# Optimization experiments

Measured on AMD Instinct MI355X. Metric: run time of the kernel, lower is better.

## Reference

```python
import jax, jax.numpy as jnp
import numpy as np

K = 256
Q = 64
T = 500001  # length of return series r


def setup_inputs() -> dict:
    key = jax.random.key(0)
    k_r, k_b, k_w0, k_w = jax.random.split(key, 4)
    r = 0.01 * jax.random.normal(k_r, (T,), dtype=jnp.float32)
    a0 = jnp.float32(0.0)
    a1 = jnp.float32(0.0)
    raw_beta0 = jnp.float32(-4.0)
    raw_beta = (-4.0 + 0.1 * jax.random.normal(k_b, (K,))).astype(jnp.float32)
    raw_w0 = (-8.0 + 0.1 * jax.random.normal(k_w0, (K,))).astype(jnp.float32)
    raw_w = (-4.0 + 0.1 * jax.random.normal(k_w, (K, Q))).astype(jnp.float32)
    return {"r": r, "a0": a0, "a1": a1, "raw_beta0": raw_beta0,
            "raw_beta": raw_beta, "raw_w0": raw_w0, "raw_w": raw_w}


def reference(r, a0, a1, raw_beta0, raw_beta, raw_w0, raw_w):
    # AR(1) residuals
    u = r[1:] - a0 - a1 * r[:-1]          # [T-1]
    u2 = u * u                            # [T-1]
    n = u.shape[0]
    # init_u2 = unbiased variance of u2, repeated q times (torch.var default ddof=1)
    init_u2 = jnp.full((Q,), jnp.var(u2, ddof=1), dtype=u2.dtype)
    u2_full = jnp.concatenate([init_u2, u2])  # [q + T-1]
    # vectorized windowing: row t holds u2_full[t+q-1], ..., u2_full[t] (flipped window)
    t_idx = jnp.arange(n)[:, None]        # [n,1]
    lag_idx = jnp.arange(Q)[None, :]      # [1,q]
    idx = (Q + t_idx) - 1 - lag_idx       # [n,q]
    u2_lags = u2_full[idx]                # [n,q]
    # softplus-MLP volatility
    w0 = jax.nn.softplus(raw_w0)          # [k]
    w = jax.nn.softplus(raw_w)            # [k,q]
    h = jax.nn.relu(w0[None, :] + u2_lags @ w.T)  # [n,k]
    beta0 = jax.nn.softplus(raw_beta0)
    beta = jax.nn.softplus(raw_beta)      # [k]
    sigma2 = beta0 + h @ beta + 1e-8      # [n]
    # Gaussian negative log-likelihood
    nll = (0.5 * n * jnp.log(jnp.float32(2.0 * np.pi))
           + 0.5 * jnp.sum(jnp.log(sigma2))
           + 0.5 * jnp.sum(u2 / sigma2))
    return nll
```

## Files before the change

### kernel.cpp

```cpp
#include <hip/hip_runtime.h>
#include <math.h>

#define K_ 256
#define Q_ 64
#define NT 500000
#define NTILES (NT / 16)
#define TT_ 16
#define NBLK ((NT + 255) / 256)
#define GRID_MAIN ((NTILES + TT_ - 1) / TT_)
#define PREP_THREADS (16384 + 2 * K_)
#define PREP_BLOCKS ((PREP_THREADS + 255) / 256)

#define WS_BETA0  2
#define WS_U2B0   4
#define WS_U2B1   (WS_U2B0 + (Q_ + NT + 1) / 2)
#define WS_BPACK  (WS_U2B1 + (Q_ + NT + 1) / 2)
#define WS_W0     (WS_BPACK + 8192)
#define WS_BETA   (WS_W0 + K_)
#define WS_PART   (WS_BETA + K_)
#define WS_PART2  (WS_PART + 2048)
#define WS_OUT    (WS_PART2 + 2048)

typedef __attribute__((ext_vector_type(8))) __bf16 bf16x8;
typedef __attribute__((ext_vector_type(4))) float  f32x4;

__device__ __forceinline__ float softplusf(float x) {
    return (x > 20.f) ? x : log1pf(__expf(x));
}

__device__ __forceinline__ unsigned short f2bf(float f) {
    unsigned int u = __float_as_uint(f);
    u = u + 0x7FFFu + ((u >> 16) & 1u);
    return (unsigned short)(u >> 16);
}

__global__ void k_front(const float* __restrict__ r,
                        const float* __restrict__ a0p,
                        const float* __restrict__ a1p,
                        const float* __restrict__ raw_beta0,
                        const float* __restrict__ raw_beta,
                        const float* __restrict__ raw_w0,
                        const float* __restrict__ raw_w,
                        float* __restrict__ ws) {
    __shared__ float red[8];
    int bi = blockIdx.x - NBLK;
    if (bi < 0) {
        int i = blockIdx.x * blockDim.x + threadIdx.x;
        float a0 = a0p[0], a1 = a1p[0];
        float v = 0.f, v2 = 0.f;
        if (i < NT) {
            float u  = r[i + 1] - a0 - a1 * r[i];
            float u2 = u * u;
            unsigned short b = f2bf(u2);
            ((unsigned short*)(ws + WS_U2B0))[Q_ + i]     = b;
            ((unsigned short*)(ws + WS_U2B1))[Q_ + i - 1] = b;
            v = u2; v2 = u2 * u2;
        }
        #pragma unroll
        for (int off = 32; off > 0; off >>= 1) {
            v  += __shfl_down(v,  off, 64);
            v2 += __shfl_down(v2, off, 64);
        }
        int wv = threadIdx.x >> 6;
        if ((threadIdx.x & 63) == 0) { red[wv * 2] = v; red[wv * 2 + 1] = v2; }
        __syncthreads();
        if (threadIdx.x == 0) {
            ws[WS_PART  + blockIdx.x] = red[0] + red[2] + red[4] + red[6];
            ws[WS_PART2 + blockIdx.x] = red[1] + red[3] + red[5] + red[7];
        }
    } else {
        int idx = bi * 256 + threadIdx.x;
        if (idx < 16384) {
            int jj = idx & 7, l = (idx >> 3) & 63, s = (idx >> 9) & 1, kc = idx >> 10;
            int j    = 32 * s + 8 * (l >> 4) + jj;
            int kout = kc * 16 + (l & 15);
            ((unsigned short*)(ws + WS_BPACK))[idx] =
                f2bf(softplusf(raw_w[kout * Q_ + (Q_ - 1 - j)]));
        } else if (idx < 16384 + K_) {
            int k = idx - 16384;
            ws[WS_W0 + k] = softplusf(raw_w0[k]);
            if (k == 0) ws[WS_BETA0] = softplusf(raw_beta0[0]);
        } else if (idx < 16384 + 2 * K_) {
            int k = idx - (16384 + K_);
            ws[WS_BETA + k] = softplusf(raw_beta[k]);
        }
    }
}

__launch_bounds__(256, 4)
__global__ void k_main(const float* __restrict__ r,
                       const float* __restrict__ a0p,
                       const float* __restrict__ a1p,
                       float* __restrict__ ws) {
    __shared__ __align__(16) float sig[TT_ * 272];
    __shared__ float red[4];

    int tid = threadIdx.x;
    int l = tid & 63, w = tid >> 6;
    int m = l & 15, q = l >> 4;

    if (blockIdx.x == 0) {
        if (tid < 64) {
            float s1 = 0.f, s2 = 0.f;
            for (int p = tid; p < NBLK; p += 64) {
                s1 += ws[WS_PART  + p];
                s2 += ws[WS_PART2 + p];
            }
            #pragma unroll
            for (int mask = 1; mask < 64; mask <<= 1) {
                s1 += __shfl_xor(s1, mask, 64);
                s2 += __shfl_xor(s2, mask, 64);
            }
            float n   = (float)NT;
            float var = (s2 - s1 * s1 / n) / (n - 1.f);
            unsigned short b = f2bf(var);
            ((unsigned short*)(ws + WS_U2B0))[tid] = b;
            if (tid < Q_ - 1) ((unsigned short*)(ws + WS_U2B1))[tid] = b;
        }
        __syncthreads();
    }

    const unsigned short* bp = (const unsigned short*)(ws + WS_BPACK);
    float beta0v = ws[WS_BETA0];
    float a0 = a0p[0], a1 = a1p[0];

    bf16x8 Wf[4][2];
    f32x4 w0c[4], betc[4];
    #pragma unroll
    for (int i = 0; i < 4; ++i) {
        int kc = w * 4 + i;
        #pragma unroll
        for (int s = 0; s < 2; ++s)
            __builtin_memcpy(&Wf[i][s], bp + ((kc * 2 + s) * 64 + l) * 8, 16);
        w0c[i]  = *(const f32x4*)(ws + WS_W0   + kc * 16 + q * 4);
        betc[i] = *(const f32x4*)(ws + WS_BETA + kc * 16 + q * 4);
    }

    int par = m & 1;
    const char* abase = (const char*)(ws + (par ? WS_U2B1 : WS_U2B0));
    int tile0 = blockIdx.x * TT_;
    int aoff = (tile0 * 16 + m + 8 * q - par) * 2;

    bf16x8 U0, U1, U0n, U1n;
    __builtin_memcpy(&U0, abase + aoff, 16);
    __builtin_memcpy(&U1, abase + aoff + 64, 16);

    #pragma unroll 2
    for (int it = 0; it < TT_; ++it) {
        int anext = aoff + 32;
        __builtin_memcpy(&U0n, abase + anext, 16);
        __builtin_memcpy(&U1n, abase + anext + 64, 16);

        float p[4];
        #pragma unroll
        for (int i = 0; i < 4; ++i) {
            f32x4 acc = __builtin_amdgcn_mfma_f32_16x16x32_bf16(Wf[i][0], U0, w0c[i], 0, 0, 0);
            acc = __builtin_amdgcn_mfma_f32_16x16x32_bf16(Wf[i][1], U1, acc, 0, 0, 0);
            float pi;
            pi = betc[i][0] * fmaxf(acc[0], 0.f);
            pi = fmaf(betc[i][1], fmaxf(acc[1], 0.f), pi);
            pi = fmaf(betc[i][2], fmaxf(acc[2], 0.f), pi);
            pi = fmaf(betc[i][3], fmaxf(acc[3], 0.f), pi);
            p[i] = pi;
        }
        sig[it * 272 + tid] = (p[0] + p[1]) + (p[2] + p[3]);

        aoff = anext; U0 = U0n; U1 = U1n;
    }

    __syncthreads();

    int tile = tid >> 4, tt = tid & 15;
    const float* sp = &sig[tile * 272 + tt];
    float s = 0.f;
    #pragma unroll
    for (int wq = 0; wq < 16; ++wq) s += sp[wq * 16];
    float sg = beta0v + s + 1e-8f;
    int t = tile0 * 16 + tid;
    float val = 0.f;
    if (t < NT) {
        float u = r[t + 1] - a0 - a1 * r[t];
        val = __logf(sg) + u * u / sg;
    }

    #pragma unroll
    for (int mask = 1; mask < 64; mask <<= 1)
        val += __shfl_xor(val, mask, 64);
    if (l == 0) red[w] = val;
    __syncthreads();
    if (tid == 0)
        ws[WS_OUT + blockIdx.x] = red[0] + red[1] + red[2] + red[3];
}

__global__ void k_final(const float* __restrict__ ws, float* __restrict__ out) {
    __shared__ float red[4];
    int tid = threadIdx.x;
    float s = 0.f;
    for (int p = tid; p < GRID_MAIN; p += 256) s += ws[WS_OUT + p];
    #pragma unroll
    for (int mask = 1; mask < 64; mask <<= 1)
        s += __shfl_xor(s, mask, 64);
    if ((tid & 63) == 0) red[tid >> 6] = s;
    __syncthreads();
    if (tid == 0)
        out[0] = 0.5f * (float)NT * 1.8378770664093453f
               + 0.5f * (red[0] + red[1] + red[2] + red[3]);
}

extern "C" void kernel_launch(void* const* d_in, const int* in_sizes, int n_in,
                              void* d_out, int out_size, void* d_ws, size_t ws_size,
                              hipStream_t stream) {
    const float* r        = (const float*)d_in[0];
    const float* a0       = (const float*)d_in[1];
    const float* a1       = (const float*)d_in[2];
    const float* raw_b0   = (const float*)d_in[3];
    const float* raw_beta = (const float*)d_in[4];
    const float* raw_w0   = (const float*)d_in[5];
    const float* raw_w    = (const float*)d_in[6];
    float* out = (float*)d_out;
    float* ws  = (float*)d_ws;

    k_front<<<NBLK + PREP_BLOCKS, 256, 0, stream>>>(
        r, a0, a1, raw_b0, raw_beta, raw_w0, raw_w, ws);

    k_main<<<GRID_MAIN, 256, 0, stream>>>(r, a0, a1, ws);

    k_final<<<1, 256, 0, stream>>>(ws, out);
}
```

Baseline: 91.13 us.

## Switch main MFMA from 16x16x32 to 32x32x16 bf16 tiles

Reworks the main kernel to compute 32-timestep by 32-hidden-unit tiles with the 32x32x16 bf16 MFMA. Each wave now covers 64 hidden units across four K-steps, and the weight packing in the prep kernel is changed to match the new operand layout. Larger tiles mean fewer cross-lane partial sums and better operand reuse per instruction. In exchange, each thread holds 16-wide accumulator, bias and beta vectors, so register pressure rises and launch bounds drop from 4 to 3 blocks per SM.

```diff
diff --git a/kernel.cpp b/kernel.cpp
--- a/kernel.cpp
+++ b/kernel.cpp
@@ -4,10 +4,9 @@
 #define K_ 256
 #define Q_ 64
 #define NT 500000
-#define NTILES (NT / 16)
-#define TT_ 16
+#define TPB 256
 #define NBLK ((NT + 255) / 256)
-#define GRID_MAIN ((NTILES + TT_ - 1) / TT_)
+#define GRID_MAIN ((NT + TPB - 1) / TPB)
 #define PREP_THREADS (16384 + 2 * K_)
 #define PREP_BLOCKS ((PREP_THREADS + 255) / 256)
 
@@ -21,8 +20,9 @@
 #define WS_PART2  (WS_PART + 2048)
 #define WS_OUT    (WS_PART2 + 2048)
 
-typedef __attribute__((ext_vector_type(8))) __bf16 bf16x8;
-typedef __attribute__((ext_vector_type(4))) float  f32x4;
+typedef __attribute__((ext_vector_type(8)))  __bf16 bf16x8;
+typedef __attribute__((ext_vector_type(4)))  float  f32x4;
+typedef __attribute__((ext_vector_type(16))) float  f32x16;
 
 __device__ __forceinline__ float softplusf(float x) {
     return (x > 20.f) ? x : log1pf(__expf(x));
@@ -71,9 +71,9 @@
     } else {
         int idx = bi * 256 + threadIdx.x;
         if (idx < 16384) {
-            int jj = idx & 7, l = (idx >> 3) & 63, s = (idx >> 9) & 1, kc = idx >> 10;
-            int j    = 32 * s + 8 * (l >> 4) + jj;
-            int kout = kc * 16 + (l & 15);
+            int jj = idx & 7, l = (idx >> 3) & 63, kb = (idx >> 9) & 3, kc = idx >> 11;
+            int j    = kb * 16 + 8 * (l >> 5) + jj;
+            int kout = kc * 32 + (l & 31);
             ((unsigned short*)(ws + WS_BPACK))[idx] =
                 f2bf(softplusf(raw_w[kout * Q_ + (Q_ - 1 - j)]));
         } else if (idx < 16384 + K_) {
@@ -87,17 +87,17 @@
     }
 }
 
-__launch_bounds__(256, 4)
+__launch_bounds__(256, 3)
 __global__ void k_main(const float* __restrict__ r,
                        const float* __restrict__ a0p,
                        const float* __restrict__ a1p,
                        float* __restrict__ ws) {
-    __shared__ __align__(16) float sig[TT_ * 272];
+    __shared__ __align__(16) float sig[8 * 264];
     __shared__ float red[4];
 
     int tid = threadIdx.x;
     int l = tid & 63, w = tid >> 6;
-    int m = l & 15, q = l >> 4;
+    int tl = l & 31, hi = l >> 5;
 
     if (blockIdx.x == 0) {
         if (tid < 64) {
@@ -124,59 +124,70 @@
     float beta0v = ws[WS_BETA0];
     float a0 = a0p[0], a1 = a1p[0];
 
-    bf16x8 Wf[4][2];
-    f32x4 w0c[4], betc[4];
-    #pragma unroll
-    for (int i = 0; i < 4; ++i) {
-        int kc = w * 4 + i;
-        #pragma unroll
-        for (int s = 0; s < 2; ++s)
-            __builtin_memcpy(&Wf[i][s], bp + ((kc * 2 + s) * 64 + l) * 8, 16);
-        w0c[i]  = *(const f32x4*)(ws + WS_W0   + kc * 16 + q * 4);
-        betc[i] = *(const f32x4*)(ws + WS_BETA + kc * 16 + q * 4);
-    }
-
-    int par = m & 1;
+    bf16x8 Wf[2][4];
+    f32x16 w0i[2], beti[2];
+    #pragma unroll
+    for (int i = 0; i < 2; ++i) {
+        int kc = w * 2 + i;
+        #pragma unroll
+        for (int kb = 0; kb < 4; ++kb)
+            __builtin_memcpy(&Wf[i][kb], bp + ((kc * 4 + kb) * 64 + l) * 8, 16);
+        #pragma unroll
+        for (int g = 0; g < 4; ++g) {
+            f32x4 t4 = *(const f32x4*)(ws + WS_W0   + kc * 32 + 8 * g + 4 * hi);
+            f32x4 b4 = *(const f32x4*)(ws + WS_BETA + kc * 32 + 8 * g + 4 * hi);
+            #pragma unroll
+            for (int j = 0; j < 4; ++j) {
+                w0i[i][g * 4 + j] = t4[j];
+                beti[i][g * 4 + j] = b4[j];
+            }
+        }
+    }
+
+    int par = l & 1;
     const char* abase = (const char*)(ws + (par ? WS_U2B1 : WS_U2B0));
-    int tile0 = blockIdx.x * TT_;
-    int aoff = (tile0 * 16 + m + 8 * q - par) * 2;
-
-    bf16x8 U0, U1, U0n, U1n;
-    __builtin_memcpy(&U0, abase + aoff, 16);
-    __builtin_memcpy(&U1, abase + aoff + 64, 16);
+    int t0 = blockIdx.x * TPB;
+    int aoff = (t0 + tl + 8 * hi - par) * 2;
+
+    bf16x8 U0, U1, U2, U3, Un0, Un1, Un2, Un3;
+    __builtin_memcpy(&U0, abase + aoff,      16);
+    __builtin_memcpy(&U1, abase + aoff + 32, 16);
+    __builtin_memcpy(&U2, abase + aoff + 64, 16);
+    __builtin_memcpy(&U3, abase + aoff + 96, 16);
 
     #pragma unroll 2
-    for (int it = 0; it < TT_; ++it) {
-        int anext = aoff + 32;
-        __builtin_memcpy(&U0n, abase + anext, 16);
-        __builtin_memcpy(&U1n, abase + anext + 64, 16);
-
-        float p[4];
-        #pragma unroll
-        for (int i = 0; i < 4; ++i) {
-            f32x4 acc = __builtin_amdgcn_mfma_f32_16x16x32_bf16(Wf[i][0], U0, w0c[i], 0, 0, 0);
-            acc = __builtin_amdgcn_mfma_f32_16x16x32_bf16(Wf[i][1], U1, acc, 0, 0, 0);
-            float pi;
-            pi = betc[i][0] * fmaxf(acc[0], 0.f);
-            pi = fmaf(betc[i][1], fmaxf(acc[1], 0.f), pi);
-            pi = fmaf(betc[i][2], fmaxf(acc[2], 0.f), pi);
-            pi = fmaf(betc[i][3], fmaxf(acc[3], 0.f), pi);
-            p[i] = pi;
-        }
-        sig[it * 272 + tid] = (p[0] + p[1]) + (p[2] + p[3]);
-
-        aoff = anext; U0 = U0n; U1 = U1n;
+    for (int it = 0; it < 8; ++it) {
+        int anext = aoff + 64;
+        __builtin_memcpy(&Un0, abase + anext,      16);
+        __builtin_memcpy(&Un1, abase + anext + 32, 16);
+        __builtin_memcpy(&Un2, abase + anext + 64, 16);
+        __builtin_memcpy(&Un3, abase + anext + 96, 16);
+
+        float pp = 0.f;
+        #pragma unroll
+        for (int i = 0; i < 2; ++i) {
+            f32x16 acc = __builtin_amdgcn_mfma_f32_32x32x16_bf16(Wf[i][0], U0, w0i[i], 0, 0, 0);
+            acc = __builtin_amdgcn_mfma_f32_32x32x16_bf16(Wf[i][1], U1, acc, 0, 0, 0);
+            acc = __builtin_amdgcn_mfma_f32_32x32x16_bf16(Wf[i][2], U2, acc, 0, 0, 0);
+            acc = __builtin_amdgcn_mfma_f32_32x32x16_bf16(Wf[i][3], U3, acc, 0, 0, 0);
+            #pragma unroll
+            for (int rr = 0; rr < 16; ++rr)
+                pp = fmaf(beti[i][rr], fmaxf(acc[rr], 0.f), pp);
+        }
+        sig[it * 264 + (w * 2 + hi) * 32 + tl] = pp;
+
+        aoff = anext;
+        U0 = Un0; U1 = Un1; U2 = Un2; U3 = Un3;
     }
 
     __syncthreads();
 
-    int tile = tid >> 4, tt = tid & 15;
-    const float* sp = &sig[tile * 272 + tt];
+    int tile = tid >> 5, tloc = tid & 31;
     float s = 0.f;
     #pragma unroll
-    for (int wq = 0; wq < 16; ++wq) s += sp[wq * 16];
+    for (int c = 0; c < 8; ++c) s += sig[tile * 264 + c * 32 + tloc];
     float sg = beta0v + s + 1e-8f;
-    int t = tile0 * 16 + tid;
+    int t = t0 + tid;
     float val = 0.f;
     if (t < NT) {
         float u = r[t + 1] - a0 - a1 * r[t];
```

Result: no change. 91.37 us (+0.3%).

## Collapse positive-weight ReLU MLP into a single 64-tap linear FIR filter

Applied to the files above, without the earlier changes.

The weights are softplus outputs, so they are positive, and the squared residual inputs are non-negative. The ReLU is therefore always the identity, and the two-layer MLP folds into one effective 64-tap vector v = W^T·beta plus a constant c0. A prep block computes v and c0 once, and the main kernel then evaluates sigma2 as an FP32 sliding-window dot product from shared memory. This removes the K=256 hidden-layer bf16 MFMA matmul. The front kernel also vectorizes the residual computation and stores FP32 u2 instead of duplicated bf16 copies.

```diff
diff --git a/kernel.cpp b/kernel.cpp
--- a/kernel.cpp
+++ b/kernel.cpp
@@ -4,34 +4,21 @@
 #define K_ 256
 #define Q_ 64
 #define NT 500000
-#define NTILES (NT / 16)
-#define TT_ 16
-#define NBLK ((NT + 255) / 256)
-#define GRID_MAIN ((NTILES + TT_ - 1) / TT_)
-#define PREP_THREADS (16384 + 2 * K_)
-#define PREP_BLOCKS ((PREP_THREADS + 255) / 256)
-
-#define WS_BETA0  2
-#define WS_U2B0   4
-#define WS_U2B1   (WS_U2B0 + (Q_ + NT + 1) / 2)
-#define WS_BPACK  (WS_U2B1 + (Q_ + NT + 1) / 2)
-#define WS_W0     (WS_BPACK + 8192)
-#define WS_BETA   (WS_W0 + K_)
-#define WS_PART   (WS_BETA + K_)
-#define WS_PART2  (WS_PART + 2048)
-#define WS_OUT    (WS_PART2 + 2048)
-
-typedef __attribute__((ext_vector_type(8))) __bf16 bf16x8;
-typedef __attribute__((ext_vector_type(4))) float  f32x4;
+#define TPB 1024
+#define NBLK_F 489
+#define GRID_MAIN 489
+
+#define WS_C0    2
+#define WS_U2    4
+#define WS_V     (WS_U2 + Q_ + NT)
+#define WS_PART  (WS_V + Q_)
+#define WS_PART2 (WS_PART + 512)
+#define WS_OUT   (WS_PART2 + 512)
+
+typedef __attribute__((ext_vector_type(4))) float f32x4;
 
 __device__ __forceinline__ float softplusf(float x) {
     return (x > 20.f) ? x : log1pf(__expf(x));
-}
-
-__device__ __forceinline__ unsigned short f2bf(float f) {
-    unsigned int u = __float_as_uint(f);
-    u = u + 0x7FFFu + ((u >> 16) & 1u);
-    return (unsigned short)(u >> 16);
 }
 
 __global__ void k_front(const float* __restrict__ r,
@@ -43,66 +30,86 @@
                         const float* __restrict__ raw_w,
                         float* __restrict__ ws) {
     __shared__ float red[8];
-    int bi = blockIdx.x - NBLK;
-    if (bi < 0) {
-        int i = blockIdx.x * blockDim.x + threadIdx.x;
+    __shared__ float sbeta[K_];
+    __shared__ float vpart[4][Q_];
+    __shared__ float cred[4];
+    int tid = threadIdx.x;
+
+    if (blockIdx.x < NBLK_F) {
+        int i0 = 4 * (blockIdx.x * 256 + tid);
         float a0 = a0p[0], a1 = a1p[0];
         float v = 0.f, v2 = 0.f;
-        if (i < NT) {
-            float u  = r[i + 1] - a0 - a1 * r[i];
-            float u2 = u * u;
-            unsigned short b = f2bf(u2);
-            ((unsigned short*)(ws + WS_U2B0))[Q_ + i]     = b;
-            ((unsigned short*)(ws + WS_U2B1))[Q_ + i - 1] = b;
-            v = u2; v2 = u2 * u2;
+        if (i0 + 7 <= NT) {
+            f32x4 ra = *(const f32x4*)(r + i0);
+            f32x4 rb = *(const f32x4*)(r + i0 + 4);
+            float u0 = ra[1] - a0 - a1 * ra[0];
+            float u1 = ra[2] - a0 - a1 * ra[1];
+            float u2 = ra[3] - a0 - a1 * ra[2];
+            float u3 = rb[0] - a0 - a1 * ra[3];
+            f32x4 q; q[0] = u0*u0; q[1] = u1*u1; q[2] = u2*u2; q[3] = u3*u3;
+            *(f32x4*)(ws + WS_U2 + Q_ + i0) = q;
+            v  = (q[0] + q[1]) + (q[2] + q[3]);
+            v2 = (q[0]*q[0] + q[1]*q[1]) + (q[2]*q[2] + q[3]*q[3]);
+        } else {
+            #pragma unroll
+            for (int j = 0; j < 4; ++j) {
+                int i = i0 + j;
+                if (i < NT) {
+                    float u = r[i + 1] - a0 - a1 * r[i];
+                    float q = u * u;
+                    ws[WS_U2 + Q_ + i] = q;
+                    v += q; v2 += q * q;
+                }
+            }
         }
         #pragma unroll
         for (int off = 32; off > 0; off >>= 1) {
             v  += __shfl_down(v,  off, 64);
             v2 += __shfl_down(v2, off, 64);
         }
-        int wv = threadIdx.x >> 6;
-        if ((threadIdx.x & 63) == 0) { red[wv * 2] = v; red[wv * 2 + 1] = v2; }
-        __syncthreads();
-        if (threadIdx.x == 0) {
+        int wv = tid >> 6;
+        if ((tid & 63) == 0) { red[wv * 2] = v; red[wv * 2 + 1] = v2; }
+        __syncthreads();
+        if (tid == 0) {
             ws[WS_PART  + blockIdx.x] = red[0] + red[2] + red[4] + red[6];
             ws[WS_PART2 + blockIdx.x] = red[1] + red[3] + red[5] + red[7];
         }
     } else {
-        int idx = bi * 256 + threadIdx.x;
-        if (idx < 16384) {
-            int jj = idx & 7, l = (idx >> 3) & 63, s = (idx >> 9) & 1, kc = idx >> 10;
-            int j    = 32 * s + 8 * (l >> 4) + jj;
-            int kout = kc * 16 + (l & 15);
-            ((unsigned short*)(ws + WS_BPACK))[idx] =
-                f2bf(softplusf(raw_w[kout * Q_ + (Q_ - 1 - j)]));
-        } else if (idx < 16384 + K_) {
-            int k = idx - 16384;
-            ws[WS_W0 + k] = softplusf(raw_w0[k]);
-            if (k == 0) ws[WS_BETA0] = softplusf(raw_beta0[0]);
-        } else if (idx < 16384 + 2 * K_) {
-            int k = idx - (16384 + K_);
-            ws[WS_BETA + k] = softplusf(raw_beta[k]);
-        }
+        sbeta[tid] = softplusf(raw_beta[tid]);
+        __syncthreads();
+        int c = tid >> 6, j = tid & 63;
+        float pv = 0.f;
+        for (int k = 64 * c; k < 64 * (c + 1); ++k)
+            pv += sbeta[k] * softplusf(raw_w[k * Q_ + j]);
+        vpart[c][j] = pv;
+        float pc = sbeta[tid] * softplusf(raw_w0[tid]);
+        #pragma unroll
+        for (int mask = 1; mask < 64; mask <<= 1)
+            pc += __shfl_xor(pc, mask, 64);
+        if (j == 0) cred[c] = pc;
+        __syncthreads();
+        if (tid < Q_) {
+            float vj = (vpart[0][tid] + vpart[1][tid])
+                     + (vpart[2][tid] + vpart[3][tid]);
+            ws[WS_V + (Q_ - 1 - tid)] = vj;
+        }
+        if (tid == 0)
+            ws[WS_C0] = softplusf(raw_beta0[0])
+                      + ((cred[0] + cred[1]) + (cred[2] + cred[3])) + 1e-8f;
     }
 }
 
-__launch_bounds__(256, 4)
-__global__ void k_main(const float* __restrict__ r,
-                       const float* __restrict__ a0p,
-                       const float* __restrict__ a1p,
-                       float* __restrict__ ws) {
-    __shared__ __align__(16) float sig[TT_ * 272];
+__launch_bounds__(256)
+__global__ void k_main(float* __restrict__ ws) {
+    __shared__ __align__(16) float su[TPB + Q_];
     __shared__ float red[4];
-
     int tid = threadIdx.x;
     int l = tid & 63, w = tid >> 6;
-    int m = l & 15, q = l >> 4;
 
     if (blockIdx.x == 0) {
         if (tid < 64) {
             float s1 = 0.f, s2 = 0.f;
-            for (int p = tid; p < NBLK; p += 64) {
+            for (int p = tid; p < NBLK_F; p += 64) {
                 s1 += ws[WS_PART  + p];
                 s2 += ws[WS_PART2 + p];
             }
@@ -113,75 +120,45 @@
             }
             float n   = (float)NT;
             float var = (s2 - s1 * s1 / n) / (n - 1.f);
-            unsigned short b = f2bf(var);
-            ((unsigned short*)(ws + WS_U2B0))[tid] = b;
-            if (tid < Q_ - 1) ((unsigned short*)(ws + WS_U2B1))[tid] = b;
+            ws[WS_U2 + tid] = var;
         }
         __syncthreads();
     }
 
-    const unsigned short* bp = (const unsigned short*)(ws + WS_BPACK);
-    float beta0v = ws[WS_BETA0];
-    float a0 = a0p[0], a1 = a1p[0];
-
-    bf16x8 Wf[4][2];
-    f32x4 w0c[4], betc[4];
-    #pragma unroll
-    for (int i = 0; i < 4; ++i) {
-        int kc = w * 4 + i;
+    int t0 = blockIdx.x * TPB;
+    for (int m = tid; m < (TPB + Q_) / 4; m += 256)
+        *(f32x4*)(su + 4 * m) = *(const f32x4*)(ws + WS_U2 + t0 + 4 * m);
+
+    float c0v = ws[WS_C0];
+    f32x4 vr4[16];
+    #pragma unroll
+    for (int m = 0; m < 16; ++m)
+        vr4[m] = *(const f32x4*)(ws + WS_V + 4 * m);
+    __syncthreads();
+
+    f32x4 acc; acc[0] = c0v; acc[1] = c0v; acc[2] = c0v; acc[3] = c0v;
+    const float* sw = su + 4 * tid;
+    f32x4 cur = *(const f32x4*)sw;
+    #pragma unroll
+    for (int m = 0; m < 16; ++m) {
+        f32x4 nxt = *(const f32x4*)(sw + 4 * m + 4);
         #pragma unroll
-        for (int s = 0; s < 2; ++s)
-            __builtin_memcpy(&Wf[i][s], bp + ((kc * 2 + s) * 64 + l) * 8, 16);
-        w0c[i]  = *(const f32x4*)(ws + WS_W0   + kc * 16 + q * 4);
-        betc[i] = *(const f32x4*)(ws + WS_BETA + kc * 16 + q * 4);
+        for (int d = 0; d < 4; ++d) {
+            float vv = vr4[m][d];
+            acc[0] = fmaf(cur[d], vv, acc[0]);
+            acc[1] = fmaf(d < 3 ? cur[d + 1] : nxt[d - 3], vv, acc[1]);
+            acc[2] = fmaf(d < 2 ? cur[d + 2] : nxt[d - 2], vv, acc[2]);
+            acc[3] = fmaf(d < 1 ? cur[d + 3] : nxt[d - 1], vv, acc[3]);
+        }
+        cur = nxt;
     }
 
-    int par = m & 1;
-    const char* abase = (const char*)(ws + (par ? WS_U2B1 : WS_U2B0));
-    int tile0 = blockIdx.x * TT_;
-    int aoff = (tile0 * 16 + m + 8 * q - par) * 2;
-
-    bf16x8 U0, U1, U0n, U1n;
-    __builtin_memcpy(&U0, abase + aoff, 16);
-    __builtin_memcpy(&U1, abase + aoff + 64, 16);
-
-    #pragma unroll 2
-    for (int it = 0; it < TT_; ++it) {
-        int anext = aoff + 32;
-        __builtin_memcpy(&U0n, abase + anext, 16);
-        __builtin_memcpy(&U1n, abase + anext + 64, 16);
-
-        float p[4];
-        #pragma unroll
-        for (int i = 0; i < 4; ++i) {
-            f32x4 acc = __builtin_amdgcn_mfma_f32_16x16x32_bf16(Wf[i][0], U0, w0c[i], 0, 0, 0);
-            acc = __builtin_amdgcn_mfma_f32_16x16x32_bf16(Wf[i][1], U1, acc, 0, 0, 0);
-            float pi;
-            pi = betc[i][0] * fmaxf(acc[0], 0.f);
-            pi = fmaf(betc[i][1], fmaxf(acc[1], 0.f), pi);
-            pi = fmaf(betc[i][2], fmaxf(acc[2], 0.f), pi);
-            pi = fmaf(betc[i][3], fmaxf(acc[3], 0.f), pi);
-            p[i] = pi;
-        }
-        sig[it * 272 + tid] = (p[0] + p[1]) + (p[2] + p[3]);
-
-        aoff = anext; U0 = U0n; U1 = U1n;
-    }
-
-    __syncthreads();
-
-    int tile = tid >> 4, tt = tid & 15;
-    const float* sp = &sig[tile * 272 + tt];
-    float s = 0.f;
-    #pragma unroll
-    for (int wq = 0; wq < 16; ++wq) s += sp[wq * 16];
-    float sg = beta0v + s + 1e-8f;
-    int t = tile0 * 16 + tid;
+    int t = t0 + 4 * tid;
+    f32x4 u4 = *(const f32x4*)(ws + WS_U2 + Q_ + t);
     float val = 0.f;
-    if (t < NT) {
-        float u = r[t + 1] - a0 - a1 * r[t];
-        val = __logf(sg) + u * u / sg;
-    }
+    #pragma unroll
+    for (int j = 0; j < 4; ++j)
+        if (t + j < NT) val += __logf(acc[j]) + u4[j] / acc[j];
 
     #pragma unroll
     for (int mask = 1; mask < 64; mask <<= 1)
@@ -189,7 +166,7 @@
     if (l == 0) red[w] = val;
     __syncthreads();
     if (tid == 0)
-        ws[WS_OUT + blockIdx.x] = red[0] + red[1] + red[2] + red[3];
+        ws[WS_OUT + blockIdx.x] = (red[0] + red[1]) + (red[2] + red[3]);
 }
 
 __global__ void k_final(const float* __restrict__ ws, float* __restrict__ out) {
@@ -204,7 +181,7 @@
     __syncthreads();
     if (tid == 0)
         out[0] = 0.5f * (float)NT * 1.8378770664093453f
-               + 0.5f * (red[0] + red[1] + red[2] + red[3]);
+               + 0.5f * ((red[0] + red[1]) + (red[2] + red[3]));
 }
 
 extern "C" void kernel_launch(void* const* d_in, const int* in_sizes, int n_in,
@@ -220,10 +197,10 @@
     float* out = (float*)d_out;
     float* ws  = (float*)d_ws;
 
-    k_front<<<NBLK + PREP_BLOCKS, 256, 0, stream>>>(
+    k_front<<<NBLK_F + 1, 256, 0, stream>>>(
         r, a0, a1, raw_b0, raw_beta, raw_w0, raw_w, ws);
 
-    k_main<<<GRID_MAIN, 256, 0, stream>>>(r, a0, a1, ws);
+    k_main<<<GRID_MAIN, 256, 0, stream>>>(ws);
 
     k_final<<<1, 256, 0, stream>>>(ws, out);
 }
```

New measurement: 107.0 us. +17.5%, slower.
